# Kernel optimization log

Hardware: AMD Instinct MI355X
Metric: run time of the kernel (lower is better)

Reference implementation:

```python
import jax, jax.numpy as jnp
import numpy as np

N = 50000
E = 800000
T = 5            # towers
F = 10           # in_num / F_in per tower (divide_input=False)
F_OUT = 2        # out_channels // towers
G = 64           # number of graphs in the batch
L = 2            # conv layers
BN_EPS = 1e-5
STD_EPS = 1e-5


def setup_inputs() -> dict:
    key = jax.random.key(0)
    ks = jax.random.split(key, 24)
    s = 0.1
    inp = {
        'x': jax.random.normal(ks[0], (N, F), jnp.float32),
        'edge_emb': jax.random.normal(ks[1], (4, F), jnp.float32) * s,
        'mlp1_w1': jax.random.normal(ks[2], (F, 5), jnp.float32) * s,
        'mlp1_b1': jnp.zeros((5,), jnp.float32),
        'mlp1_w2': jax.random.normal(ks[3], (5, F), jnp.float32) * s,
        'mlp1_b2': jnp.zeros((F,), jnp.float32),
        'enc_w': jax.random.normal(ks[4], (L, F, F), jnp.float32) * s,
        'enc_b': jnp.zeros((L, F), jnp.float32),
        'pre_w': jax.random.normal(ks[5], (L, T, 3 * F, F), jnp.float32) * s,
        'pre_b': jnp.zeros((L, T, F), jnp.float32),
        'post_w': jax.random.normal(ks[6], (L, T, 13 * F, F_OUT), jnp.float32) * s,
        'post_b': jnp.zeros((L, T, F_OUT), jnp.float32),
        'lin_w': jax.random.normal(ks[7], (L, F, F), jnp.float32) * s,
        'lin_b': jnp.zeros((L, F), jnp.float32),
        'bn_gamma': jnp.ones((L, F), jnp.float32),
        'bn_beta': jnp.zeros((L, F), jnp.float32),
        'mlp2_w1': jax.random.normal(ks[8], (F, 5), jnp.float32) * s,
        'mlp2_b1': jnp.zeros((5,), jnp.float32),
        'mlp2_w2': jax.random.normal(ks[9], (5, 1), jnp.float32) * s,
        'mlp2_b2': jnp.zeros((1,), jnp.float32),
        'edge_index': jax.random.randint(ks[10], (2, E), 0, N, jnp.int64),
        'edge_attr': jax.random.randint(ks[11], (E,), 0, 4, jnp.int64),
        'batch': jnp.sort(jax.random.randint(ks[12], (N,), 0, G, jnp.int64)),
    }
    return inp


def reference(x, edge_emb, mlp1_w1, mlp1_b1, mlp1_w2, mlp1_b2,
              enc_w, enc_b, pre_w, pre_b, post_w, post_b, lin_w, lin_b,
              bn_gamma, bn_beta, mlp2_w1, mlp2_b1, mlp2_w2, mlp2_b2,
              edge_index, edge_attr, batch):
    src, dst = edge_index[0], edge_index[1]
    # mlp1: 10 -> 5 -> 10
    h = jax.nn.relu(x @ mlp1_w1 + mlp1_b1) @ mlp1_w2 + mlp1_b2  # [N, F]
    ea = edge_emb[edge_attr]  # [E, F] edge embedding lookup

    # in-degree at target nodes, PNA degree statistics
    deg = jax.ops.segment_sum(jnp.ones((src.shape[0],), h.dtype), dst, num_segments=N)
    d = jnp.clip(deg, 1.0)
    avg_log = jnp.mean(jnp.log(deg + 1.0))  # avg_deg['log'] from degree distribution
    log_d = jnp.log(d + 1.0)
    amp = (log_d / avg_log)[:, None, None]
    att = (avg_log / log_d)[:, None, None]
    has_in = (deg > 0)[:, None, None]
    inv_d = (1.0 / d)[:, None, None]

    for l in range(L):
        e = ea @ enc_w[l] + enc_b[l]  # [E, F]
        # message = pre_nn(cat(x_i, x_j, edge_attr)) per tower (x shared across towers)
        msg_in = jnp.concatenate([h[dst], h[src], e], axis=-1)  # [E, 3F]
        m = jnp.einsum('ef,tfo->eto', msg_in, pre_w[l]) + pre_b[l]  # [E, T, F]
        mean = jax.ops.segment_sum(m, dst, num_segments=N) * inv_d
        mean2 = jax.ops.segment_sum(m * m, dst, num_segments=N) * inv_d
        std = jnp.sqrt(jax.nn.relu(mean2 - mean * mean) + STD_EPS)
        mn = jnp.where(has_in, jax.ops.segment_min(m, dst, num_segments=N), 0.0)
        mx = jnp.where(has_in, jax.ops.segment_max(m, dst, num_segments=N), 0.0)
        agg = jnp.concatenate([mean, mn, mx, std], axis=-1)  # [N, T, 4F]
        agg = jnp.concatenate([agg, agg * amp, agg * att], axis=-1)  # [N, T, 12F]
        xt = jnp.broadcast_to(h[:, None, :], (h.shape[0], T, F))
        o = jnp.concatenate([xt, agg], axis=-1)  # [N, T, 13F]
        o = jnp.einsum('ntf,tfo->nto', o, post_w[l]) + post_b[l]  # [N, T, F_OUT]
        o = o.reshape(o.shape[0], T * F_OUT) @ lin_w[l] + lin_b[l]  # [N, F]
        # train-mode BatchNorm over nodes
        mu = jnp.mean(o, axis=0)
        var = jnp.var(o, axis=0)
        o = (o - mu) / jnp.sqrt(var + BN_EPS) * bn_gamma[l] + bn_beta[l]
        h = jax.nn.relu(o)

    g = jax.ops.segment_sum(h, batch, num_segments=G)  # global_add_pool -> [G, F]
    out = jax.nn.relu(g @ mlp2_w1 + mlp2_b1) @ mlp2_w2 + mlp2_b2  # [G, 1]
    return out
```

## Files before the change

kernel.cpp:

```cpp
#include <hip/hip_runtime.h>
#include <hip/hip_fp16.h>
#include <math.h>

#define N_NODES 50000
#define N_EDGES 800000
#define G_GRAPHS 64
#define BSTRIDE 64
#define UROW 64
#define SENPK (N_NODES * 128)
#define SBLK 512
#define EPB 1563
#define NBUCK 1563
#define SCAP 12

#define WAVE_SYNC() asm volatile("s_waitcnt lgkmcnt(0)" ::: "memory")
#define RFL(v) __builtin_amdgcn_readfirstlane(v)

__global__ __launch_bounds__(256) void k_front(
    const float* __restrict__ x,
    const float* __restrict__ w1, const float* __restrict__ b1,
    const float* __restrict__ w2, const float* __restrict__ b2,
    float* __restrict__ h,
    float* __restrict__ bn_part, float* __restrict__ g,
    float* __restrict__ avg_log,
    const float* __restrict__ edge_emb,
    const float* __restrict__ enc_w, const float* __restrict__ enc_b,
    const float* __restrict__ pre_w, float* __restrict__ encm,
    __half* __restrict__ u,
    const int* __restrict__ src, const int* __restrict__ dst,
    const int* __restrict__ attr,
    int* __restrict__ rec,
    unsigned char* __restrict__ cntmat) {
  __shared__ int hist[NBUCK];
  __shared__ float eo[2][4][10];
  __shared__ float sw[500];
  int tid = threadIdx.x, blk = blockIdx.x;
  int gid = blk * 256 + tid;

  for (int i = tid; i < NBUCK; i += 256) hist[i] = 0;
  for (int j = tid; j < 500; j += 256) {
    int t = j / 100, k = (j / 10) % 10, f = j % 10;
    sw[j] = pre_w[(t * 30 + 10 + k) * 10 + f];
  }
  if (blk == 0) {
    for (int i = tid; i < 80; i += 256) {
      int l = i / 40; int a = (i / 10) % 4; int k = i % 10;
      float s = enc_b[l * 10 + k];
      for (int j = 0; j < 10; j++) s += edge_emb[a * 10 + j] * enc_w[(l * 10 + j) * 10 + k];
      eo[l][a][k] = s;
    }
  }
  if (gid < 1280) bn_part[gid] = 0.f;
  if (gid >= 1280 && gid < 1280 + G_GRAPHS * 10) g[gid - 1280] = 0.f;
  if (gid == 0) avg_log[0] = 0.f;
  { int z = gid - 2048; if (z >= 0 && z < UROW) u[(size_t)N_NODES * UROW + z] = __float2half(0.f); }
  __syncthreads();

  int ebase = blk * EPB;
  for (int i = tid; i < EPB; i += 256) {
    int e = ebase + i;
    if (e < N_EDGES) {
      int d = dst[e];
      int s = src[e];
      int a = attr[e];
      int bkt = d >> 5;
      int r = atomicAdd(&hist[bkt], 1);
      if (r < SCAP) rec[(bkt * SBLK + blk) * SCAP + r] = (s * 128 + a) | ((d & 31) << 23);
    }
  }

  if (gid < N_NODES) {
    const float2* xp = (const float2*)(x + gid * 10);
    float xv[10];
#pragma unroll
    for (int k = 0; k < 5; k++) { float2 v = xp[k]; xv[2 * k] = v.x; xv[2 * k + 1] = v.y; }
    float hid[5];
#pragma unroll
    for (int j = 0; j < 5; j++) {
      float a = b1[j];
#pragma unroll
      for (int k = 0; k < 10; k++) a += xv[k] * w1[k * 5 + j];
      hid[j] = fmaxf(a, 0.f);
    }
    float hr[10];
#pragma unroll
    for (int f = 0; f < 10; f++) {
      float a = b2[f];
#pragma unroll
      for (int j = 0; j < 5; j++) a += hid[j] * w2[j * 10 + f];
      hr[f] = a;
      h[gid * 10 + f] = a;
    }
    __half2* up = (__half2*)(u + (size_t)gid * UROW);
#pragma unroll
    for (int c0 = 0; c0 < 25; c0++) {
      int ca = 2 * c0, cb = 2 * c0 + 1;
      int ta = ca / 10, fa = ca % 10, tb = cb / 10, fb = cb % 10;
      float a = 0.f, b = 0.f;
#pragma unroll
      for (int k = 0; k < 10; k++) {
        a += hr[k] * sw[ta * 100 + fa + k * 10];
        b += hr[k] * sw[tb * 100 + fb + k * 10];
      }
      up[c0] = __floats2half2_rn(a, b);
    }
  }

  if (blk == 0) {
    for (int i = tid; i < 400; i += 256) {
      int l = i / 200; int a = (i / 50) % 4; int t = (i / 10) % 5; int f = i % 10;
      float s = 0.f;
      for (int k = 0; k < 10; k++) s += eo[l][a][k] * pre_w[((l * 5 + t) * 30 + 20 + k) * 10 + f];
      encm[i] = s;
    }
  }
  __syncthreads();
  for (int b2 = tid; b2 < NBUCK; b2 += 256) {
    int c = hist[b2];
    cntmat[(size_t)blk * NBUCK + b2] = (unsigned char)(c < SCAP ? c : SCAP);
  }
}

__global__ __launch_bounds__(256) void k_bucket(
    const int* __restrict__ rec, const unsigned char* __restrict__ cntmat,
    int* __restrict__ epk, int* __restrict__ cnt,
    float* __restrict__ avg_log) {
  __shared__ int lc[SBLK];
  __shared__ int lcnt[32];
  int tid = threadIdx.x, b = blockIdx.x;
  for (int s = tid; s < SBLK; s += 256) lc[s] = cntmat[(size_t)s * NBUCK + b];
  if (tid < 32) lcnt[tid] = 0;
  __syncthreads();
  const int* rb = rec + (size_t)b * SBLK * SCAP;
#pragma unroll
  for (int p = 0; p < (SBLK * SCAP) / 256; p++) {
    int t2 = tid + p * 256;
    int j = t2 / SCAP, i = t2 % SCAP;
    if (i < lc[j]) {
      int r = rb[t2];
      int d5 = r >> 23;
      int rank = atomicAdd(&lcnt[d5], 1);
      if (rank < BSTRIDE) epk[((b << 5) + d5) * BSTRIDE + rank] = r & 0x7FFFFF;
    }
  }
  __syncthreads();
  float acc = 0.f;
  if (tid < 32) {
    int node = (b << 5) + tid;
    if (node < N_NODES) {
      int dg = lcnt[tid];
      cnt[node] = dg;
      if (dg > BSTRIDE) dg = BSTRIDE;
      acc = __logf((float)dg + 1.f);
    }
  }
  if (tid < 64) {
#pragma unroll
    for (int d = 32; d >= 1; d >>= 1) acc += __shfl_down(acc, d, 64);
    if (tid == 0) atomicAdd(avg_log, acc);
  }
}

__global__ __launch_bounds__(256) void k_conv(
    const float* __restrict__ h,
    const __half* __restrict__ u,
    const float* __restrict__ pre_w_l,
    const float* __restrict__ pre_b_l,
    const float* __restrict__ post_w_l,
    const float* __restrict__ post_b_l,
    const float* __restrict__ lin_w_l,
    const float* __restrict__ lin_b_l,
    const float* __restrict__ encm_l,
    const int* __restrict__ cnt,
    const int* __restrict__ epk,
    const float* __restrict__ avg_log_p,
    float* __restrict__ o_buf,
    float* __restrict__ bn_part)
{
  __shared__ float sW[1300];
  __shared__ float sLin[100];
  __shared__ float sLb[10];
  __shared__ float sPb[10];
  __shared__ float sP[4][100];
  __shared__ float sO[4][10];
  __shared__ float bnS[10], bnQ[10];

  int tid = threadIdx.x;
  int wid = RFL(tid >> 6);
  int lane = tid & 63;
  for (int i = tid; i < 1300; i += 256) sW[i] = post_w_l[i];
  for (int i = tid; i < 100; i += 256) sLin[i] = lin_w_l[i];
  if (tid < 10) {
    sLb[tid] = lin_b_l[tid];
    sPb[tid] = post_b_l[tid];
    bnS[tid] = 0.f; bnQ[tid] = 0.f;
  }
  __syncthreads();

  int f = lane % 10;
  int t = (lane < 50) ? (lane / 10) : 4;
  int c50 = t * 10 + f;
  const char* ub = (const char*)u;
  int c50_2 = c50 * 2;
  float wdst[10];
#pragma unroll
  for (int k = 0; k < 10; k++) wdst[k] = pre_w_l[(t * 30 + k) * 10 + f];
  float em0 = encm_l[c50];
  float em1 = encm_l[50 + c50];
  float em2 = encm_l[100 + c50];
  float em3 = encm_l[150 + c50];
  float preb = pre_b_l[c50];
  float avg_log = avg_log_p[0] * (1.f / N_NODES);

  int n = blockIdx.x * 4 + wid;
  float bnSv = 0.f, bnQv = 0.f;

#define PRE(US, AS, IDX) { int sp_ = __builtin_amdgcn_readlane(pk, (IDX) & 63); \
    AS = sp_ & 3; \
    US = __half2float(*(const __half*)(ub + (sp_ & ~7) + c50_2)); }
#define PROC(US, AS) { float m_ = ((AS & 2) ? ((AS & 1) ? bem3 : bem2) : ((AS & 1) ? bem1 : bem0)) + US; \
    sum += m_; sq = fmaf(m_, m_, sq); mnv = fminf(mnv, m_); mxv = fmaxf(mxv, m_); }

  if (n < N_NODES) {
    int deg = RFL(cnt[n]);
    if (deg > BSTRIDE) deg = BSTRIDE;
    int pk = epk[n * BSTRIDE + lane];
    pk = (lane < deg) ? pk : SENPK;

    const float* hn = h + n * 10;
    float2 d0 = *(const float2*)hn;
    float2 d1 = *(const float2*)(hn + 2);
    float2 d2 = *(const float2*)(hn + 4);
    float2 d3 = *(const float2*)(hn + 6);
    float2 d4 = *(const float2*)(hn + 8);
    float xf = hn[f];

    float base = preb
      + d0.x * wdst[0] + d0.y * wdst[1] + d1.x * wdst[2] + d1.y * wdst[3]
      + d2.x * wdst[4] + d2.y * wdst[5] + d3.x * wdst[6] + d3.y * wdst[7]
      + d4.x * wdst[8] + d4.y * wdst[9];
    float bem0 = base + em0, bem1 = base + em1, bem2 = base + em2, bem3 = base + em3;

    float sum = 0.f, sq = 0.f, mnv = INFINITY, mxv = -INFINITY;
    {
      float u0, u1, u2, u3, u4, u5, u6, u7;
      int a0, a1, a2, a3, a4, a5, a6, a7;
      PRE(u0, a0, 0) PRE(u1, a1, 1) PRE(u2, a2, 2) PRE(u3, a3, 3)
      PRE(u4, a4, 4) PRE(u5, a5, 5) PRE(u6, a6, 6) PRE(u7, a7, 7)
      int full = deg & ~7;
      int jb = 0;
      for (; jb < full; jb += 8) {
        PROC(u0, a0) PRE(u0, a0, jb + 8)
        PROC(u1, a1) PRE(u1, a1, jb + 9)
        PROC(u2, a2) PRE(u2, a2, jb + 10)
        PROC(u3, a3) PRE(u3, a3, jb + 11)
        PROC(u4, a4) PRE(u4, a4, jb + 12)
        PROC(u5, a5) PRE(u5, a5, jb + 13)
        PROC(u6, a6) PRE(u6, a6, jb + 14)
        PROC(u7, a7) PRE(u7, a7, jb + 15)
      }
      if (jb + 0 < deg) PROC(u0, a0)
      if (jb + 1 < deg) PROC(u1, a1)
      if (jb + 2 < deg) PROC(u2, a2)
      if (jb + 3 < deg) PROC(u3, a3)
      if (jb + 4 < deg) PROC(u4, a4)
      if (jb + 5 < deg) PROC(u5, a5)
      if (jb + 6 < deg) PROC(u6, a6)
    }

    float degf = (float)deg;
    float d = fmaxf(degf, 1.f);
    float inv = 1.f / d;
    float mean = sum * inv;
    float var = sq * inv - mean * mean;
    float stdv = sqrtf(fmaxf(var, 0.f) + 1e-5f);
    if (deg == 0) { mnv = 0.f; mxv = 0.f; }
    float log_d = logf(d + 1.f);
    float amp = log_d / avg_log;
    float att = avg_log / log_d;

    float vv[13];
    vv[0] = xf;
    vv[1] = mean;       vv[2] = mnv;        vv[3] = mxv;        vv[4] = stdv;
    vv[5] = mean * amp; vv[6] = mnv * amp;  vv[7] = mxv * amp;  vv[8] = stdv * amp;
    vv[9] = mean * att; vv[10] = mnv * att; vv[11] = mxv * att; vv[12] = stdv * att;
    float p0 = 0.f, p1 = 0.f;
#pragma unroll
    for (int j = 0; j < 13; j++) {
      const float2 w = *(const float2*)&sW[t * 260 + (f + 10 * j) * 2];
      p0 += vv[j] * w.x; p1 += vv[j] * w.y;
    }
    if (lane < 50) *(float2*)&sP[wid][c50 * 2] = make_float2(p0, p1);
    WAVE_SYNC();
    if (lane < 10) {
      int tt = lane >> 1, c = lane & 1;
      float o = sPb[lane];
#pragma unroll
      for (int ff = 0; ff < 10; ff++) o += sP[wid][(tt * 10 + ff) * 2 + c];
      sO[wid][lane] = o;
    }
    WAVE_SYNC();
    if (lane < 10) {
      float r = sLb[lane];
#pragma unroll
      for (int j = 0; j < 10; j++) r += sO[wid][j] * sLin[j * 10 + lane];
      o_buf[n * 10 + lane] = r;
      bnSv = r; bnQv = r * r;
    }
  }
#undef PRE
#undef PROC

  if (lane < 10) {
    atomicAdd(&bnS[lane], bnSv);
    atomicAdd(&bnQ[lane], bnQv);
  }
  __syncthreads();
  if (tid < 20) {
    float v = (tid < 10) ? bnS[tid] : bnQ[tid - 10];
    atomicAdd(&bn_part[(blockIdx.x & 31) * 20 + tid], v);
  }
}

__global__ __launch_bounds__(256) void k_bnpool(
    const float* __restrict__ o_buf,
    const float* __restrict__ bn_part,
    const float* __restrict__ gamma, const float* __restrict__ beta,
    float* __restrict__ h,
    const int* __restrict__ batch, float* __restrict__ g,
    const float* __restrict__ pre_w_next, __half* __restrict__ u,
    int do_u, int do_pool) {
  __shared__ float sS[20];
  __shared__ float sMu[10], sInv[10];
  __shared__ float pool[8][10];
  __shared__ float hrow[25][10];
  __shared__ float sw[500];
  __shared__ int g0s;
  int tid = threadIdx.x;
  int n0 = blockIdx.x * 25;
  if (do_u) {
    for (int j = tid; j < 500; j += 256) {
      int t = j / 100, k = (j / 10) % 10, f = j % 10;
      sw[j] = pre_w_next[(t * 30 + 10 + k) * 10 + f];
    }
  }
  if (tid < 20) {
    float s = 0.f;
    for (int j = 0; j < 32; j++) s += bn_part[j * 20 + tid];
    sS[tid] = s;
  }
  if (tid < 80) pool[tid / 10][tid % 10] = 0.f;
  if (tid == 0) g0s = batch[n0];
  __syncthreads();
  if (tid < 10) {
    float mu = sS[tid] * (1.f / N_NODES);
    float var = sS[10 + tid] * (1.f / N_NODES) - mu * mu;
    sMu[tid] = mu;
    sInv[tid] = 1.f / sqrtf(fmaxf(var, 0.f) + 1e-5f);
  }
  __syncthreads();
  if (tid < 250) {
    int dn = tid / 10, f = tid % 10;
    int n = n0 + dn;
    int i = n * 10 + f;
    float o = (o_buf[i] - sMu[f]) * sInv[f] * gamma[f] + beta[f];
    float r = fmaxf(o, 0.f);
    h[i] = r;
    hrow[dn][f] = r;
    if (do_pool) {
      int dg = batch[n] - g0s;
      if (dg < 8) atomicAdd(&pool[dg][f], r);
      else atomicAdd(&g[(g0s + dg) * 10 + f], r);
    }
  }
  __syncthreads();
  if (do_u && tid < 250) {
#pragma unroll
    for (int it = 0; it < 5; it++) {
      int j = tid + it * 250;
      int node = j / 50, c = j % 50;
      int t = c / 10, f2 = c % 10;
      float acc = 0.f;
#pragma unroll
      for (int k = 0; k < 10; k++) acc += hrow[node][k] * sw[t * 100 + f2 + k * 10];
      u[(size_t)(n0 + node) * UROW + c] = __float2half_rn(acc);
    }
  }
  if (do_pool) {
    __syncthreads();
    if (tid < 80) {
      float v = pool[tid / 10][tid % 10];
      if (v != 0.f) atomicAdd(&g[(g0s + tid / 10) * 10 + tid % 10], v);
    }
  }
}

__global__ void k_mlp2(const float* __restrict__ g,
                       const float* __restrict__ w1, const float* __restrict__ b1,
                       const float* __restrict__ w2, const float* __restrict__ b2,
                       float* __restrict__ out) {
  int b = threadIdx.x;
  if (b >= G_GRAPHS) return;
  float gv[10];
#pragma unroll
  for (int k = 0; k < 10; k++) gv[k] = g[b * 10 + k];
  float acc = b2[0];
#pragma unroll
  for (int j = 0; j < 5; j++) {
    float a = b1[j];
#pragma unroll
    for (int k = 0; k < 10; k++) a += gv[k] * w1[k * 5 + j];
    acc += fmaxf(a, 0.f) * w2[j];
  }
  out[b] = acc;
}

extern "C" void kernel_launch(void* const* d_in, const int* in_sizes, int n_in,
                              void* d_out, int out_size, void* d_ws, size_t ws_size,
                              hipStream_t stream) {
  const float* x        = (const float*)d_in[0];
  const float* edge_emb = (const float*)d_in[1];
  const float* m1w1 = (const float*)d_in[2];
  const float* m1b1 = (const float*)d_in[3];
  const float* m1w2 = (const float*)d_in[4];
  const float* m1b2 = (const float*)d_in[5];
  const float* enc_w = (const float*)d_in[6];
  const float* enc_b = (const float*)d_in[7];
  const float* pre_w = (const float*)d_in[8];
  const float* pre_b = (const float*)d_in[9];
  const float* post_w = (const float*)d_in[10];
  const float* post_b = (const float*)d_in[11];
  const float* lin_w = (const float*)d_in[12];
  const float* lin_b = (const float*)d_in[13];
  const float* bn_g = (const float*)d_in[14];
  const float* bn_b = (const float*)d_in[15];
  const float* m2w1 = (const float*)d_in[16];
  const float* m2b1 = (const float*)d_in[17];
  const float* m2w2 = (const float*)d_in[18];
  const float* m2b2 = (const float*)d_in[19];
  const int* edge_index = (const int*)d_in[20];
  const int* edge_attr  = (const int*)d_in[21];
  const int* batch      = (const int*)d_in[22];
  const int* src  = edge_index;
  const int* dstp = edge_index + N_EDGES;

  char* ws = (char*)d_ws;
  size_t off = 0;
  auto alloc = [&](size_t bytes) {
    void* p = ws + off;
    off += (bytes + 255) & ~(size_t)255;
    return p;
  };
  float*  h       = (float*)alloc(N_NODES * 10 * sizeof(float));
  float*  o_buf   = (float*)alloc(N_NODES * 10 * sizeof(float));
  __half* u       = (__half*)alloc((size_t)(N_NODES + 1) * UROW * sizeof(__half));
  int*    cnt     = (int*)alloc((size_t)N_NODES * sizeof(int));
  int*    epk     = (int*)alloc((size_t)N_NODES * BSTRIDE * sizeof(int));
  int*    rec     = (int*)alloc((size_t)NBUCK * SBLK * SCAP * sizeof(int));
  unsigned char* cntmat = (unsigned char*)alloc((size_t)SBLK * NBUCK);
  float*  encm    = (float*)alloc(400 * sizeof(float));
  float*  avg_log = (float*)alloc(16);
  float*  bn_part = (float*)alloc(2 * 32 * 20 * sizeof(float));
  float*  g       = (float*)alloc(G_GRAPHS * 10 * sizeof(float));

  k_front<<<SBLK, 256, 0, stream>>>(x, m1w1, m1b1, m1w2, m1b2, h,
                                    bn_part, g, avg_log,
                                    edge_emb, enc_w, enc_b, pre_w, encm, u,
                                    src, dstp, edge_attr, rec, cntmat);
  k_bucket<<<NBUCK, 256, 0, stream>>>(rec, cntmat, epk, cnt, avg_log);

  for (int l = 0; l < 2; l++) {
    k_conv<<<N_NODES / 4, 256, 0, stream>>>(
        h, u, pre_w + l * 1500, pre_b + l * 50, post_w + l * 1300, post_b + l * 10,
        lin_w + l * 100, lin_b + l * 10, encm + l * 200,
        cnt, epk, avg_log, o_buf, bn_part + l * 640);
    k_bnpool<<<N_NODES / 25, 256, 0, stream>>>(
        o_buf, bn_part + l * 640, bn_g + l * 10, bn_b + l * 10, h, batch, g,
        pre_w + 1500, u, l == 0, l == 1);
  }
  k_mlp2<<<1, 64, 0, stream>>>(g, m2w1, m2b1, m2w2, m2b2, (float*)d_out);
}
```

Measured before the change: 280.0 us.

## Fold edge-attribute embedding into per-node u table, fuse mlp2 into last bnpool

Stores four precomputed variants of each node's projected features in u, one per edge attribute, with the attribute embedding already added. Each edge gather therefore indexes directly by (src,attr) and the per-edge attribute select disappears from the conv inner loop. Other changes: epk padding is written in k_bucket instead of masking per lane, fast reciprocal/log intrinsics are used, and the mlp2 launch is removed by a last-block ticket inside k_bnpool. The cost is a u table four times larger, so u writes and cache footprint grow.

```diff
diff --git a/kernel.cpp b/kernel.cpp
--- a/kernel.cpp
+++ b/kernel.cpp
@@ -7,7 +7,7 @@
 #define G_GRAPHS 64
 #define BSTRIDE 64
 #define UROW 64
-#define SENPK (N_NODES * 128)
+#define SENPK (N_NODES * 512)
 #define SBLK 512
 #define EPB 1563
 #define NBUCK 1563
@@ -22,17 +22,18 @@
     const float* __restrict__ w2, const float* __restrict__ b2,
     float* __restrict__ h,
     float* __restrict__ bn_part, float* __restrict__ g,
-    float* __restrict__ avg_log,
+    float* __restrict__ avg_log, int* __restrict__ ticket,
     const float* __restrict__ edge_emb,
     const float* __restrict__ enc_w, const float* __restrict__ enc_b,
-    const float* __restrict__ pre_w, float* __restrict__ encm,
+    const float* __restrict__ pre_w,
     __half* __restrict__ u,
     const int* __restrict__ src, const int* __restrict__ dst,
     const int* __restrict__ attr,
     int* __restrict__ rec,
     unsigned char* __restrict__ cntmat) {
   __shared__ int hist[NBUCK];
-  __shared__ float eo[2][4][10];
+  __shared__ float seo[4][10];
+  __shared__ float sEm[200];
   __shared__ float sw[500];
   int tid = threadIdx.x, blk = blockIdx.x;
   int gid = blk * 256 + tid;
@@ -42,18 +43,24 @@
     int t = j / 100, k = (j / 10) % 10, f = j % 10;
     sw[j] = pre_w[(t * 30 + 10 + k) * 10 + f];
   }
-  if (blk == 0) {
-    for (int i = tid; i < 80; i += 256) {
-      int l = i / 40; int a = (i / 10) % 4; int k = i % 10;
-      float s = enc_b[l * 10 + k];
-      for (int j = 0; j < 10; j++) s += edge_emb[a * 10 + j] * enc_w[(l * 10 + j) * 10 + k];
-      eo[l][a][k] = s;
-    }
+  for (int i = tid; i < 40; i += 256) {
+    int a = i / 10, k = i % 10;
+    float s = enc_b[k];
+    for (int j = 0; j < 10; j++) s += edge_emb[a * 10 + j] * enc_w[j * 10 + k];
+    seo[a][k] = s;
   }
   if (gid < 1280) bn_part[gid] = 0.f;
   if (gid >= 1280 && gid < 1280 + G_GRAPHS * 10) g[gid - 1280] = 0.f;
   if (gid == 0) avg_log[0] = 0.f;
-  { int z = gid - 2048; if (z >= 0 && z < UROW) u[(size_t)N_NODES * UROW + z] = __float2half(0.f); }
+  if (gid == 1) ticket[0] = 0;
+  { int z = gid - 2048; if (z >= 0 && z < UROW) u[(size_t)N_NODES * 4 * UROW + z] = __float2half(0.f); }
+  __syncthreads();
+  for (int i = tid; i < 200; i += 256) {
+    int a = i / 50, c = i % 50, t = c / 10, f = c % 10;
+    float s = 0.f;
+    for (int k = 0; k < 10; k++) s += seo[a][k] * pre_w[(t * 30 + 20 + k) * 10 + f];
+    sEm[i] = s;
+  }
   __syncthreads();
 
   int ebase = blk * EPB;
@@ -65,7 +72,7 @@
       int a = attr[e];
       int bkt = d >> 5;
       int r = atomicAdd(&hist[bkt], 1);
-      if (r < SCAP) rec[(bkt * SBLK + blk) * SCAP + r] = (s * 128 + a) | ((d & 31) << 23);
+      if (r < SCAP) rec[(bkt * SBLK + blk) * SCAP + r] = (s * 4 + a) | ((d & 31) << 18);
     }
   }
 
@@ -91,7 +98,7 @@
       hr[f] = a;
       h[gid * 10 + f] = a;
     }
-    __half2* up = (__half2*)(u + (size_t)gid * UROW);
+    __half2* up = (__half2*)(u) + (size_t)gid * 128;
 #pragma unroll
     for (int c0 = 0; c0 < 25; c0++) {
       int ca = 2 * c0, cb = 2 * c0 + 1;
@@ -102,18 +109,12 @@
         a += hr[k] * sw[ta * 100 + fa + k * 10];
         b += hr[k] * sw[tb * 100 + fb + k * 10];
       }
-      up[c0] = __floats2half2_rn(a, b);
-    }
-  }
-
-  if (blk == 0) {
-    for (int i = tid; i < 400; i += 256) {
-      int l = i / 200; int a = (i / 50) % 4; int t = (i / 10) % 5; int f = i % 10;
-      float s = 0.f;
-      for (int k = 0; k < 10; k++) s += eo[l][a][k] * pre_w[((l * 5 + t) * 30 + 20 + k) * 10 + f];
-      encm[i] = s;
-    }
-  }
+#pragma unroll
+      for (int at = 0; at < 4; at++)
+        up[at * 32 + c0] = __floats2half2_rn(a + sEm[at * 50 + ca], b + sEm[at * 50 + cb]);
+    }
+  }
+
   __syncthreads();
   for (int b2 = tid; b2 < NBUCK; b2 += 256) {
     int c = hist[b2];
@@ -138,9 +139,9 @@
     int j = t2 / SCAP, i = t2 % SCAP;
     if (i < lc[j]) {
       int r = rb[t2];
-      int d5 = r >> 23;
+      int d5 = r >> 18;
       int rank = atomicAdd(&lcnt[d5], 1);
-      if (rank < BSTRIDE) epk[((b << 5) + d5) * BSTRIDE + rank] = r & 0x7FFFFF;
+      if (rank < BSTRIDE) epk[((b << 5) + d5) * BSTRIDE + rank] = (r & 0x3FFFF) << 7;
     }
   }
   __syncthreads();
@@ -151,6 +152,8 @@
       int dg = lcnt[tid];
       cnt[node] = dg;
       if (dg > BSTRIDE) dg = BSTRIDE;
+      int pe = dg + 8 < BSTRIDE ? dg + 8 : BSTRIDE;
+      for (int j = dg; j < pe; j++) epk[node * BSTRIDE + j] = SENPK;
       acc = __logf((float)dg + 1.f);
     }
   }
@@ -170,7 +173,6 @@
     const float* __restrict__ post_b_l,
     const float* __restrict__ lin_w_l,
     const float* __restrict__ lin_b_l,
-    const float* __restrict__ encm_l,
     const int* __restrict__ cnt,
     const int* __restrict__ epk,
     const float* __restrict__ avg_log_p,
@@ -205,27 +207,22 @@
   float wdst[10];
 #pragma unroll
   for (int k = 0; k < 10; k++) wdst[k] = pre_w_l[(t * 30 + k) * 10 + f];
-  float em0 = encm_l[c50];
-  float em1 = encm_l[50 + c50];
-  float em2 = encm_l[100 + c50];
-  float em3 = encm_l[150 + c50];
   float preb = pre_b_l[c50];
   float avg_log = avg_log_p[0] * (1.f / N_NODES);
+  float ainv = __builtin_amdgcn_rcpf(avg_log);
 
   int n = blockIdx.x * 4 + wid;
   float bnSv = 0.f, bnQv = 0.f;
 
-#define PRE(US, AS, IDX) { int sp_ = __builtin_amdgcn_readlane(pk, (IDX) & 63); \
-    AS = sp_ & 3; \
-    US = __half2float(*(const __half*)(ub + (sp_ & ~7) + c50_2)); }
-#define PROC(US, AS) { float m_ = ((AS & 2) ? ((AS & 1) ? bem3 : bem2) : ((AS & 1) ? bem1 : bem0)) + US; \
+#define PRE(US, IDX) { int sp_ = __builtin_amdgcn_readlane(pk, (IDX) & 63); \
+    US = __half2float(*(const __half*)(ub + sp_ + c50_2)); }
+#define PROC(US) { float m_ = base + US; \
     sum += m_; sq = fmaf(m_, m_, sq); mnv = fminf(mnv, m_); mxv = fmaxf(mxv, m_); }
 
   if (n < N_NODES) {
+    int pk = epk[n * BSTRIDE + lane];
     int deg = RFL(cnt[n]);
     if (deg > BSTRIDE) deg = BSTRIDE;
-    int pk = epk[n * BSTRIDE + lane];
-    pk = (lane < deg) ? pk : SENPK;
 
     const float* hn = h + n * 10;
     float2 d0 = *(const float2*)hn;
@@ -239,45 +236,43 @@
       + d0.x * wdst[0] + d0.y * wdst[1] + d1.x * wdst[2] + d1.y * wdst[3]
       + d2.x * wdst[4] + d2.y * wdst[5] + d3.x * wdst[6] + d3.y * wdst[7]
       + d4.x * wdst[8] + d4.y * wdst[9];
-    float bem0 = base + em0, bem1 = base + em1, bem2 = base + em2, bem3 = base + em3;
 
     float sum = 0.f, sq = 0.f, mnv = INFINITY, mxv = -INFINITY;
     {
       float u0, u1, u2, u3, u4, u5, u6, u7;
-      int a0, a1, a2, a3, a4, a5, a6, a7;
-      PRE(u0, a0, 0) PRE(u1, a1, 1) PRE(u2, a2, 2) PRE(u3, a3, 3)
-      PRE(u4, a4, 4) PRE(u5, a5, 5) PRE(u6, a6, 6) PRE(u7, a7, 7)
+      PRE(u0, 0) PRE(u1, 1) PRE(u2, 2) PRE(u3, 3)
+      PRE(u4, 4) PRE(u5, 5) PRE(u6, 6) PRE(u7, 7)
       int full = deg & ~7;
       int jb = 0;
       for (; jb < full; jb += 8) {
-        PROC(u0, a0) PRE(u0, a0, jb + 8)
-        PROC(u1, a1) PRE(u1, a1, jb + 9)
-        PROC(u2, a2) PRE(u2, a2, jb + 10)
-        PROC(u3, a3) PRE(u3, a3, jb + 11)
-        PROC(u4, a4) PRE(u4, a4, jb + 12)
-        PROC(u5, a5) PRE(u5, a5, jb + 13)
-        PROC(u6, a6) PRE(u6, a6, jb + 14)
-        PROC(u7, a7) PRE(u7, a7, jb + 15)
+        PROC(u0) PRE(u0, jb + 8)
+        PROC(u1) PRE(u1, jb + 9)
+        PROC(u2) PRE(u2, jb + 10)
+        PROC(u3) PRE(u3, jb + 11)
+        PROC(u4) PRE(u4, jb + 12)
+        PROC(u5) PRE(u5, jb + 13)
+        PROC(u6) PRE(u6, jb + 14)
+        PROC(u7) PRE(u7, jb + 15)
       }
-      if (jb + 0 < deg) PROC(u0, a0)
-      if (jb + 1 < deg) PROC(u1, a1)
-      if (jb + 2 < deg) PROC(u2, a2)
-      if (jb + 3 < deg) PROC(u3, a3)
-      if (jb + 4 < deg) PROC(u4, a4)
-      if (jb + 5 < deg) PROC(u5, a5)
-      if (jb + 6 < deg) PROC(u6, a6)
+      if (jb + 0 < deg) PROC(u0)
+      if (jb + 1 < deg) PROC(u1)
+      if (jb + 2 < deg) PROC(u2)
+      if (jb + 3 < deg) PROC(u3)
+      if (jb + 4 < deg) PROC(u4)
+      if (jb + 5 < deg) PROC(u5)
+      if (jb + 6 < deg) PROC(u6)
     }
 
     float degf = (float)deg;
     float d = fmaxf(degf, 1.f);
-    float inv = 1.f / d;
+    float inv = __builtin_amdgcn_rcpf(d);
     float mean = sum * inv;
     float var = sq * inv - mean * mean;
     float stdv = sqrtf(fmaxf(var, 0.f) + 1e-5f);
     if (deg == 0) { mnv = 0.f; mxv = 0.f; }
-    float log_d = logf(d + 1.f);
-    float amp = log_d / avg_log;
-    float att = avg_log / log_d;
+    float log_d = __logf(d + 1.f);
+    float amp = log_d * ainv;
+    float att = avg_log * __builtin_amdgcn_rcpf(log_d);
 
     float vv[13];
     vv[0] = xf;
@@ -329,13 +324,22 @@
     float* __restrict__ h,
     const int* __restrict__ batch, float* __restrict__ g,
     const float* __restrict__ pre_w_next, __half* __restrict__ u,
+    const float* __restrict__ edge_emb,
+    const float* __restrict__ enc_w, const float* __restrict__ enc_b,
+    const float* __restrict__ m2w1, const float* __restrict__ m2b1,
+    const float* __restrict__ m2w2, const float* __restrict__ m2b2,
+    int* __restrict__ ticket, float* __restrict__ out,
     int do_u, int do_pool) {
   __shared__ float sS[20];
   __shared__ float sMu[10], sInv[10];
   __shared__ float pool[8][10];
   __shared__ float hrow[25][10];
   __shared__ float sw[500];
+  __shared__ float seo[4][10];
+  __shared__ float sEm[200];
+  __shared__ float usl[1250];
   __shared__ int g0s;
+  __shared__ int amLast;
   int tid = threadIdx.x;
   int n0 = blockIdx.x * 25;
   if (do_u) {
@@ -343,6 +347,12 @@
       int t = j / 100, k = (j / 10) % 10, f = j % 10;
       sw[j] = pre_w_next[(t * 30 + 10 + k) * 10 + f];
     }
+    for (int i = tid; i < 40; i += 256) {
+      int a = i / 10, k = i % 10;
+      float s = enc_b[10 + k];
+      for (int j = 0; j < 10; j++) s += edge_emb[a * 10 + j] * enc_w[(10 + j) * 10 + k];
+      seo[a][k] = s;
+    }
   }
   if (tid < 20) {
     float s = 0.f;
@@ -352,6 +362,14 @@
   if (tid < 80) pool[tid / 10][tid % 10] = 0.f;
   if (tid == 0) g0s = batch[n0];
   __syncthreads();
+  if (do_u) {
+    for (int i = tid; i < 200; i += 256) {
+      int a = i / 50, c = i % 50, t = c / 10, f = c % 10;
+      float s = 0.f;
+      for (int k = 0; k < 10; k++) s += seo[a][k] * pre_w_next[(t * 30 + 20 + k) * 10 + f];
+      sEm[i] = s;
+    }
+  }
   if (tid < 10) {
     float mu = sS[tid] * (1.f / N_NODES);
     float var = sS[10 + tid] * (1.f / N_NODES) - mu * mu;
@@ -374,16 +392,30 @@
     }
   }
   __syncthreads();
-  if (do_u && tid < 250) {
-#pragma unroll
-    for (int it = 0; it < 5; it++) {
-      int j = tid + it * 250;
-      int node = j / 50, c = j % 50;
-      int t = c / 10, f2 = c % 10;
-      float acc = 0.f;
-#pragma unroll
-      for (int k = 0; k < 10; k++) acc += hrow[node][k] * sw[t * 100 + f2 + k * 10];
-      u[(size_t)(n0 + node) * UROW + c] = __float2half_rn(acc);
+  if (do_u) {
+    if (tid < 250) {
+#pragma unroll
+      for (int it = 0; it < 5; it++) {
+        int j = tid + it * 250;
+        int node = j / 50, c = j % 50;
+        int t = c / 10, f2 = c % 10;
+        float acc = 0.f;
+#pragma unroll
+        for (int k = 0; k < 10; k++) acc += hrow[node][k] * sw[t * 100 + f2 + k * 10];
+        usl[j] = acc;
+      }
+    }
+    __syncthreads();
+    if (tid < 250) {
+#pragma unroll
+      for (int it = 0; it < 10; it++) {
+        int j2 = tid + it * 250;
+        int node = j2 / 100, rem = j2 % 100;
+        int a = rem / 25, c0 = rem % 25;
+        float va = usl[node * 50 + 2 * c0] + sEm[a * 50 + 2 * c0];
+        float vb = usl[node * 50 + 2 * c0 + 1] + sEm[a * 50 + 2 * c0 + 1];
+        ((__half2*)u)[((size_t)(n0 + node) * 4 + a) * 32 + c0] = __floats2half2_rn(va, vb);
+      }
     }
   }
   if (do_pool) {
@@ -392,27 +424,25 @@
       float v = pool[tid / 10][tid % 10];
       if (v != 0.f) atomicAdd(&g[(g0s + tid / 10) * 10 + tid % 10], v);
     }
-  }
-}
-
-__global__ void k_mlp2(const float* __restrict__ g,
-                       const float* __restrict__ w1, const float* __restrict__ b1,
-                       const float* __restrict__ w2, const float* __restrict__ b2,
-                       float* __restrict__ out) {
-  int b = threadIdx.x;
-  if (b >= G_GRAPHS) return;
-  float gv[10];
-#pragma unroll
-  for (int k = 0; k < 10; k++) gv[k] = g[b * 10 + k];
-  float acc = b2[0];
-#pragma unroll
-  for (int j = 0; j < 5; j++) {
-    float a = b1[j];
-#pragma unroll
-    for (int k = 0; k < 10; k++) a += gv[k] * w1[k * 5 + j];
-    acc += fmaxf(a, 0.f) * w2[j];
-  }
-  out[b] = acc;
+    __threadfence();
+    __syncthreads();
+    if (tid == 0) amLast = (atomicAdd(ticket, 1) == (int)gridDim.x - 1);
+    __syncthreads();
+    if (amLast && tid < G_GRAPHS) {
+      float gv[10];
+#pragma unroll
+      for (int k = 0; k < 10; k++) gv[k] = atomicAdd(&g[tid * 10 + k], 0.f);
+      float acc = m2b2[0];
+#pragma unroll
+      for (int j = 0; j < 5; j++) {
+        float a = m2b1[j];
+#pragma unroll
+        for (int k = 0; k < 10; k++) a += gv[k] * m2w1[k * 5 + j];
+        acc += fmaxf(a, 0.f) * m2w2[j];
+      }
+      out[tid] = acc;
+    }
+  }
 }
 
 extern "C" void kernel_launch(void* const* d_in, const int* in_sizes, int n_in,
@@ -453,30 +483,31 @@
   };
   float*  h       = (float*)alloc(N_NODES * 10 * sizeof(float));
   float*  o_buf   = (float*)alloc(N_NODES * 10 * sizeof(float));
-  __half* u       = (__half*)alloc((size_t)(N_NODES + 1) * UROW * sizeof(__half));
+  __half* u       = (__half*)alloc(((size_t)N_NODES * 4 + 1) * UROW * sizeof(__half));
   int*    cnt     = (int*)alloc((size_t)N_NODES * sizeof(int));
   int*    epk     = (int*)alloc((size_t)N_NODES * BSTRIDE * sizeof(int));
   int*    rec     = (int*)alloc((size_t)NBUCK * SBLK * SCAP * sizeof(int));
   unsigned char* cntmat = (unsigned char*)alloc((size_t)SBLK * NBUCK);
-  float*  encm    = (float*)alloc(400 * sizeof(float));
   float*  avg_log = (float*)alloc(16);
+  int*    ticket  = (int*)alloc(16);
   float*  bn_part = (float*)alloc(2 * 32 * 20 * sizeof(float));
   float*  g       = (float*)alloc(G_GRAPHS * 10 * sizeof(float));
 
   k_front<<<SBLK, 256, 0, stream>>>(x, m1w1, m1b1, m1w2, m1b2, h,
-                                    bn_part, g, avg_log,
-                                    edge_emb, enc_w, enc_b, pre_w, encm, u,
+                                    bn_part, g, avg_log, ticket,
+                                    edge_emb, enc_w, enc_b, pre_w, u,
                                     src, dstp, edge_attr, rec, cntmat);
   k_bucket<<<NBUCK, 256, 0, stream>>>(rec, cntmat, epk, cnt, avg_log);
 
   for (int l = 0; l < 2; l++) {
     k_conv<<<N_NODES / 4, 256, 0, stream>>>(
         h, u, pre_w + l * 1500, pre_b + l * 50, post_w + l * 1300, post_b + l * 10,
-        lin_w + l * 100, lin_b + l * 10, encm + l * 200,
+        lin_w + l * 100, lin_b + l * 10,
         cnt, epk, avg_log, o_buf, bn_part + l * 640);
     k_bnpool<<<N_NODES / 25, 256, 0, stream>>>(
         o_buf, bn_part + l * 640, bn_g + l * 10, bn_b + l * 10, h, batch, g,
-        pre_w + 1500, u, l == 0, l == 1);
-  }
-  k_mlp2<<<1, 64, 0, stream>>>(g, m2w1, m2b1, m2w2, m2b2, (float*)d_out);
+        pre_w + 1500, u, edge_emb, enc_w, enc_b,
+        m2w1, m2b1, m2w2, m2b2, ticket, (float*)d_out,
+        l == 0, l == 1);
+  }
 }
```

New measurement: 399.9 us. 1.43x slower.
